# Optimization experiments

Measured on AMD Instinct MI355X. Metric: run time of the kernel, lower is better.

The kernel has to match this reference:

```python
import jax, jax.numpy as jnp
import numpy as np


def setup_inputs() -> dict:
    key = jax.random.key(0)
    k0, k1, k2, k3, k4 = jax.random.split(key, 5)
    feat0 = jax.random.normal(k0, (32, 256, 56, 56), dtype=jnp.float32)
    feat1 = jax.random.normal(k1, (32, 512, 28, 28), dtype=jnp.float32)
    feat2 = jax.random.normal(k2, (32, 1024, 14, 14), dtype=jnp.float32)
    feat3 = jax.random.normal(k3, (32, 2048, 7, 7), dtype=jnp.float32)
    # Conv2d(3840 -> 1024, kernel_size=1, bias=False): weight [emb, C_total]
    conv_w = jax.random.normal(k4, (1024, 3840), dtype=jnp.float32) * 0.02
    return {"feat0": feat0, "feat1": feat1, "feat2": feat2, "feat3": feat3, "conv_w": conv_w}


def reference(feat0, feat1, feat2, feat3, conv_w):
    # Target spatial size = earliest (largest) level.
    Ht, Wt = feat0.shape[2], feat0.shape[3]

    def up_mean(f):
        # Bilinear upsample (torch Upsample align_corners=False == jax 'bilinear'
        # half-pixel resize), then spatial mean per channel.  Because the 1x1
        # conv and global avg-pool are linear, pooling each upsampled level
        # first and applying the conv on the pooled vector is exactly the
        # same math as conv(concat(upsampled)) followed by avg-pool.
        B, C = f.shape[0], f.shape[1]
        up = jax.image.resize(f, (B, C, Ht, Wt), method='bilinear')  # [B,C,Ht,Wt]
        return jnp.mean(up, axis=(2, 3))  # [B,C]

    v = jnp.concatenate([up_mean(f) for f in (feat0, feat1, feat2, feat3)], axis=1)  # [B, 3840]
    # 1x1 conv (no bias) on pooled vector == GEMM with conv weight, then squeeze.
    return v @ conv_w.T  # [B, emb]
```

## Files before the change

kernel.cpp:

```cpp
#include <hip/hip_runtime.h>


#define AS1(p) ((const __attribute__((address_space(1))) void*)(p))
#define AS3(p) ((__attribute__((address_space(3))) void*)(p))

__global__ __launch_bounds__(256) void pool_kernel(
    const float* __restrict__ f0, const float* __restrict__ f1,
    const float* __restrict__ f2, const float* __restrict__ f3,
    float* __restrict__ v)
{
    __shared__ float l[12544];
    int bid = blockIdx.x, t = threadIdx.x;
    int wave = t >> 6, lane = t & 63;

    const float* base;
    if (bid < 2048)      base = f0 + (size_t)bid * 12544;
    else if (bid < 3072) base = f1 + (size_t)(bid - 2048) * 12544;
    else if (bid < 3584) base = f2 + (size_t)(bid - 3072) * 12544;
    else                 base = f3 + (size_t)(bid - 3584) * 12544;

    {
        const float* g = base + wave * 3136;
        float* ld = l + wave * 3136;
        #pragma unroll
        for (int r = 0; r < 12; ++r) {
            __builtin_amdgcn_global_load_lds(
                AS1(g + r * 256 + lane * 4), AS3(ld + r * 256), 16, 0, 0);
        }
        if (lane < 16) {
            __builtin_amdgcn_global_load_lds(
                AS1(g + 3072 + lane * 4), AS3(ld + 3072), 16, 0, 0);
        }
    }
    asm volatile("s_waitcnt vmcnt(0)" ::: "memory");
    __syncthreads();

    const float* seg = l + t * 49;
    float s = 0.f;
    #pragma unroll
    for (int i = 0; i < 49; ++i) s += seg[i];

    if (bid < 2048) {
        #pragma unroll
        for (int o = 32; o; o >>= 1) s += __shfl_xor(s, o);
        if (lane == 0) {
            int q = bid * 4 + wave;
            v[(q >> 8) * 3840 + (q & 255)] = s * (1.f / 3136.f);
        }
    } else if (bid < 3072) {
        s += __shfl_xor(s, 8); s += __shfl_xor(s, 4);
        s += __shfl_xor(s, 2); s += __shfl_xor(s, 1);
        if ((t & 15) == 0) {
            int q = (bid - 2048) * 16 + (t >> 4);
            v[(q >> 9) * 3840 + 256 + (q & 511)] = s * (1.f / 784.f);
        }
    } else if (bid < 3584) {
        s += __shfl_xor(s, 2); s += __shfl_xor(s, 1);
        if ((t & 3) == 0) {
            int q = (bid - 3072) * 64 + (t >> 2);
            v[(q >> 10) * 3840 + 768 + (q & 1023)] = s * (1.f / 196.f);
        }
    } else {
        int q = (bid - 3584) * 256 + t;
        v[(q >> 11) * 3840 + 1792 + (q & 2047)] = s * (1.f / 49.f);
    }
}

#define KT 120

__global__ __launch_bounds__(256) void gemm_kernel(
    const float* __restrict__ v, const float* __restrict__ W,
    float* __restrict__ partials)
{
    __shared__ float vs[32][124];
    __shared__ float wsh[64][124];
    int t = threadIdx.x;
    int et = blockIdx.x & 15, ks = blockIdx.x >> 4;
    int e0 = et << 6, k0 = ks * KT;

    {
        float4 tmp[7];
        int row[7], c4[7];
        #pragma unroll
        for (int i = 0; i < 7; ++i) {
            int f = t + (i << 8);
            row[i] = f / 30; c4[i] = f % 30;
            tmp[i] = *(const float4*)&W[(size_t)(e0 + row[i]) * 3840 + k0 + c4[i] * 4];
        }
        float4 tail; int rowt = 0, c4t = 0;
        if (t < 128) {
            int f = t + 1792;
            rowt = f / 30; c4t = f % 30;
            tail = *(const float4*)&W[(size_t)(e0 + rowt) * 3840 + k0 + c4t * 4];
        }
        #pragma unroll
        for (int i = 0; i < 7; ++i)
            *(float4*)&wsh[row[i]][c4[i] * 4] = tmp[i];
        if (t < 128)
            *(float4*)&wsh[rowt][c4t * 4] = tail;
    }
    {
        float4 tmp[3];
        int row[3], c4[3];
        #pragma unroll
        for (int i = 0; i < 3; ++i) {
            int f = t + (i << 8);
            row[i] = f / 30; c4[i] = f % 30;
            tmp[i] = *(const float4*)&v[row[i] * 3840 + k0 + c4[i] * 4];
        }
        float4 tail; int rowt = 0, c4t = 0;
        if (t < 192) {
            int f = t + 768;
            rowt = f / 30; c4t = f % 30;
            tail = *(const float4*)&v[rowt * 3840 + k0 + c4t * 4];
        }
        #pragma unroll
        for (int i = 0; i < 3; ++i)
            *(float4*)&vs[row[i]][c4[i] * 4] = tmp[i];
        if (t < 192)
            *(float4*)&vs[rowt][c4t * 4] = tail;
    }
    __syncthreads();

    int bg = t >> 5, eg = t & 31;
    int b0 = bg << 2;
    float acc[4][2] = {};
    #pragma unroll 5
    for (int k = 0; k < KT; k += 4) {
        float4 vv[4], ww[2];
        #pragma unroll
        for (int i = 0; i < 4; ++i) vv[i] = *(const float4*)&vs[b0 + i][k];
        #pragma unroll
        for (int j = 0; j < 2; ++j) ww[j] = *(const float4*)&wsh[eg + (j << 5)][k];
        #pragma unroll
        for (int i = 0; i < 4; ++i)
            #pragma unroll
            for (int j = 0; j < 2; ++j)
                acc[i][j] += vv[i].x * ww[j].x + vv[i].y * ww[j].y +
                             vv[i].z * ww[j].z + vv[i].w * ww[j].w;
    }

    float* pout = partials + (size_t)ks * 32768 + (size_t)b0 * 1024 + e0 + eg;
    #pragma unroll
    for (int i = 0; i < 4; ++i)
        #pragma unroll
        for (int j = 0; j < 2; ++j)
            pout[i * 1024 + (j << 5)] = acc[i][j];
}

__global__ __launch_bounds__(256) void reduce_kernel(
    const float* __restrict__ partials, float* __restrict__ out)
{
    int idx = blockIdx.x * 256 + threadIdx.x;
    float s0 = 0.f, s1 = 0.f, s2 = 0.f, s3 = 0.f;
    #pragma unroll
    for (int sp = 0; sp < 32; sp += 4) {
        s0 += partials[(sp + 0) * 32768 + idx];
        s1 += partials[(sp + 1) * 32768 + idx];
        s2 += partials[(sp + 2) * 32768 + idx];
        s3 += partials[(sp + 3) * 32768 + idx];
    }
    out[idx] = (s0 + s1) + (s2 + s3);
}

extern "C" void kernel_launch(void* const* d_in, const int* in_sizes, int n_in,
                              void* d_out, int out_size, void* d_ws, size_t ws_size,
                              hipStream_t stream)
{
    const float* f0 = (const float*)d_in[0];
    const float* f1 = (const float*)d_in[1];
    const float* f2 = (const float*)d_in[2];
    const float* f3 = (const float*)d_in[3];
    const float* W  = (const float*)d_in[4];
    float* out = (float*)d_out;

    float* v        = (float*)d_ws;
    float* partials = v + 32 * 3840;

    pool_kernel<<<3840, 256, 0, stream>>>(f0, f1, f2, f3, v);
    gemm_kernel<<<512, 256, 0, stream>>>(v, W, partials);
    reduce_kernel<<<128, 256, 0, stream>>>(partials, out);
}
```

Before: 233.9 us.

## Make pooling kernel persistent with double-buffered LDS prefetch of channel chunks

Replaces the one-shot pooling kernel with a persistent grid of 1536 blocks. Each block walks 10 chunks of 3136 floats, prefetching the next chunk into a second LDS buffer with async global-to-LDS loads while it reduces the current one. This cuts the LDS footprint per block roughly in half, which should allow more resident blocks per CU, and it overlaps loads with the reduction. In exchange, the level-0 path now needs a cross-wave reduction through LDS plus a block barrier, and the reduction mapping becomes more complex.

```diff
diff --git a/kernel.cpp b/kernel.cpp
--- a/kernel.cpp
+++ b/kernel.cpp
@@ -9,60 +9,77 @@
     const float* __restrict__ f2, const float* __restrict__ f3,
     float* __restrict__ v)
 {
-    __shared__ float l[12544];
-    int bid = blockIdx.x, t = threadIdx.x;
-    int wave = t >> 6, lane = t & 63;
-
-    const float* base;
-    if (bid < 2048)      base = f0 + (size_t)bid * 12544;
-    else if (bid < 3072) base = f1 + (size_t)(bid - 2048) * 12544;
-    else if (bid < 3584) base = f2 + (size_t)(bid - 3072) * 12544;
-    else                 base = f3 + (size_t)(bid - 3584) * 12544;
-
-    {
-        const float* g = base + wave * 3136;
-        float* ld = l + wave * 3136;
-        #pragma unroll
-        for (int r = 0; r < 12; ++r) {
+    __shared__ float l[2 * 3136 + 8];
+    int t = threadIdx.x, w = t >> 6, lane = t & 63;
+    float* warr = l + 6272;
+
+    int c0 = blockIdx.x;
+
+    auto stage = [&](int c, int buf) {
+        const float* base;
+        if (c < 8192)       base = f0 + (size_t)c * 3136;
+        else if (c < 12288) base = f1 + (size_t)(c - 8192) * 3136;
+        else if (c < 14336) base = f2 + (size_t)(c - 12288) * 3136;
+        else                base = f3 + (size_t)(c - 14336) * 3136;
+        const float* g = base + w * 784;
+        float* ld = l + buf * 3136 + w * 784;
+        #pragma unroll
+        for (int r = 0; r < 3; ++r)
             __builtin_amdgcn_global_load_lds(
                 AS1(g + r * 256 + lane * 4), AS3(ld + r * 256), 16, 0, 0);
-        }
-        if (lane < 16) {
+        if (lane < 4)
             __builtin_amdgcn_global_load_lds(
-                AS1(g + 3072 + lane * 4), AS3(ld + 3072), 16, 0, 0);
-        }
-    }
-    asm volatile("s_waitcnt vmcnt(0)" ::: "memory");
-    __syncthreads();
-
-    const float* seg = l + t * 49;
-    float s = 0.f;
-    #pragma unroll
-    for (int i = 0; i < 49; ++i) s += seg[i];
-
-    if (bid < 2048) {
-        #pragma unroll
-        for (int o = 32; o; o >>= 1) s += __shfl_xor(s, o);
-        if (lane == 0) {
-            int q = bid * 4 + wave;
-            v[(q >> 8) * 3840 + (q & 255)] = s * (1.f / 3136.f);
-        }
-    } else if (bid < 3072) {
-        s += __shfl_xor(s, 8); s += __shfl_xor(s, 4);
-        s += __shfl_xor(s, 2); s += __shfl_xor(s, 1);
-        if ((t & 15) == 0) {
-            int q = (bid - 2048) * 16 + (t >> 4);
-            v[(q >> 9) * 3840 + 256 + (q & 511)] = s * (1.f / 784.f);
-        }
-    } else if (bid < 3584) {
-        s += __shfl_xor(s, 2); s += __shfl_xor(s, 1);
-        if ((t & 3) == 0) {
-            int q = (bid - 3072) * 64 + (t >> 2);
-            v[(q >> 10) * 3840 + 768 + (q & 1023)] = s * (1.f / 196.f);
-        }
-    } else {
-        int q = (bid - 3584) * 256 + t;
-        v[(q >> 11) * 3840 + 1792 + (q & 2047)] = s * (1.f / 49.f);
+                AS1(g + 768 + lane * 4), AS3(ld + 768), 16, 0, 0);
+    };
+
+    stage(c0, 0);
+    #pragma unroll 1
+    for (int i = 0; i < 10; ++i) {
+        int c = c0 + 1536 * i;
+        if (i < 9) {
+            stage(c0 + 1536 * (i + 1), (i + 1) & 1);
+            asm volatile("s_waitcnt vmcnt(4)" ::: "memory");
+        } else {
+            asm volatile("s_waitcnt vmcnt(0)" ::: "memory");
+        }
+
+        const float* ldb = l + (i & 1) * 3136 + w * 784;
+        const float* seg = ldb + (lane >> 2) * 49 + (lane & 3) * 12;
+        float s = 0.f;
+        #pragma unroll
+        for (int k = 0; k < 12; ++k) s += seg[k];
+        if ((lane & 3) == 3) s += seg[12];
+        s += __shfl_xor(s, 1); s += __shfl_xor(s, 2);
+
+        if (c < 8192) {
+            s += __shfl_xor(s, 4);  s += __shfl_xor(s, 8);
+            s += __shfl_xor(s, 16); s += __shfl_xor(s, 32);
+            if (lane == 0) warr[(i & 1) * 4 + w] = s;
+            __syncthreads();
+            if (t == 0) {
+                const float* wa = warr + (i & 1) * 4;
+                v[(c >> 8) * 3840 + (c & 255)] =
+                    (wa[0] + wa[1] + wa[2] + wa[3]) * (1.f / 3136.f);
+            }
+        } else if (c < 12288) {
+            s += __shfl_xor(s, 4);  s += __shfl_xor(s, 8);
+            s += __shfl_xor(s, 16); s += __shfl_xor(s, 32);
+            if (lane == 0) {
+                int q = (c - 8192) * 4 + w;
+                v[(q >> 9) * 3840 + 256 + (q & 511)] = s * (1.f / 784.f);
+            }
+        } else if (c < 14336) {
+            s += __shfl_xor(s, 4); s += __shfl_xor(s, 8);
+            if ((lane & 15) == 0) {
+                int q = (c - 12288) * 16 + w * 4 + (lane >> 4);
+                v[(q >> 10) * 3840 + 768 + (q & 1023)] = s * (1.f / 196.f);
+            }
+        } else {
+            if ((lane & 3) == 0) {
+                int q = (c - 14336) * 64 + w * 16 + (lane >> 2);
+                v[(q >> 11) * 3840 + 1792 + (q & 2047)] = s * (1.f / 49.f);
+            }
+        }
     }
 }
 
@@ -177,7 +194,7 @@
     float* v        = (float*)d_ws;
     float* partials = v + 32 * 3840;
 
-    pool_kernel<<<3840, 256, 0, stream>>>(f0, f1, f2, f3, v);
+    pool_kernel<<<1536, 256, 0, stream>>>(f0, f1, f2, f3, v);
     gemm_kernel<<<512, 256, 0, stream>>>(v, W, partials);
     reduce_kernel<<<128, 256, 0, stream>>>(partials, out);
 }
```

Result: no change. 235.9 us (+0.9%).

## Replace LDS staging in pooling kernel with direct register loads

Applied to the files above, without the earlier changes.

The pooling kernel no longer stages each 12544-float block through LDS with global_load_lds. For levels 0 and 1, each wave loads one 3136-float chunk as float4 values straight into registers. Level-1 channels are split into four per-lane partial sums and written back as a single float4. For levels 2 and 3, each thread reads its 49-element channel segment directly from global memory. Removing the 50 KB of shared memory per block should allow more blocks per CU, at the cost of strided per-thread loads on the small levels and higher register use.

```diff
diff --git a/kernel.cpp b/kernel.cpp
--- a/kernel.cpp
+++ b/kernel.cpp
@@ -1,68 +1,79 @@
 #include <hip/hip_runtime.h>
 
 
-#define AS1(p) ((const __attribute__((address_space(1))) void*)(p))
-#define AS3(p) ((__attribute__((address_space(3))) void*)(p))
+__device__ __forceinline__ float s4(float4 a) { return (a.x + a.y) + (a.z + a.w); }
 
 __global__ __launch_bounds__(256) void pool_kernel(
     const float* __restrict__ f0, const float* __restrict__ f1,
     const float* __restrict__ f2, const float* __restrict__ f3,
     float* __restrict__ v)
 {
-    __shared__ float l[12544];
-    int bid = blockIdx.x, t = threadIdx.x;
-    int wave = t >> 6, lane = t & 63;
+    int t = threadIdx.x, w = t >> 6, lane = t & 63;
+    int bid = blockIdx.x;
 
-    const float* base;
-    if (bid < 2048)      base = f0 + (size_t)bid * 12544;
-    else if (bid < 3072) base = f1 + (size_t)(bid - 2048) * 12544;
-    else if (bid < 3584) base = f2 + (size_t)(bid - 3072) * 12544;
-    else                 base = f3 + (size_t)(bid - 3584) * 12544;
+    if (bid < 3072) {
+        int chunk = bid * 4 + w;
+        const float* base = (chunk < 8192)
+            ? f0 + (size_t)chunk * 3136
+            : f1 + (size_t)(chunk - 8192) * 3136;
+        const float4* p = (const float4*)base;
+        float4 r[12];
+        #pragma unroll
+        for (int i = 0; i < 12; ++i) r[i] = p[lane + (i << 6)];
+        float4 tl = make_float4(0.f, 0.f, 0.f, 0.f);
+        if (lane < 16) tl = p[768 + lane];
 
-    {
-        const float* g = base + wave * 3136;
-        float* ld = l + wave * 3136;
-        #pragma unroll
-        for (int r = 0; r < 12; ++r) {
-            __builtin_amdgcn_global_load_lds(
-                AS1(g + r * 256 + lane * 4), AS3(ld + r * 256), 16, 0, 0);
-        }
-        if (lane < 16) {
-            __builtin_amdgcn_global_load_lds(
-                AS1(g + 3072 + lane * 4), AS3(ld + 3072), 16, 0, 0);
-        }
-    }
-    asm volatile("s_waitcnt vmcnt(0)" ::: "memory");
-    __syncthreads();
-
-    const float* seg = l + t * 49;
-    float s = 0.f;
-    #pragma unroll
-    for (int i = 0; i < 49; ++i) s += seg[i];
-
-    if (bid < 2048) {
-        #pragma unroll
-        for (int o = 32; o; o >>= 1) s += __shfl_xor(s, o);
-        if (lane == 0) {
-            int q = bid * 4 + wave;
-            v[(q >> 8) * 3840 + (q & 255)] = s * (1.f / 3136.f);
-        }
-    } else if (bid < 3072) {
-        s += __shfl_xor(s, 8); s += __shfl_xor(s, 4);
-        s += __shfl_xor(s, 2); s += __shfl_xor(s, 1);
-        if ((t & 15) == 0) {
-            int q = (bid - 2048) * 16 + (t >> 4);
-            v[(q >> 9) * 3840 + 256 + (q & 511)] = s * (1.f / 784.f);
-        }
-    } else if (bid < 3584) {
-        s += __shfl_xor(s, 2); s += __shfl_xor(s, 1);
-        if ((t & 3) == 0) {
-            int q = (bid - 3072) * 64 + (t >> 2);
-            v[(q >> 10) * 3840 + 768 + (q & 1023)] = s * (1.f / 196.f);
+        if (chunk < 8192) {
+            float s = 0.f;
+            #pragma unroll
+            for (int i = 0; i < 12; ++i) s += s4(r[i]);
+            s += s4(tl);
+            #pragma unroll
+            for (int o = 32; o; o >>= 1) s += __shfl_xor(s, o);
+            if (lane == 0)
+                v[(chunk >> 8) * 3840 + (chunk & 255)] = s * (1.f / 3136.f);
+        } else {
+            float a0 = s4(r[0]) + s4(r[1]) + s4(r[2]) + (lane <  4 ? s4(r[3]) : 0.f);
+            float a1 = (lane <  4 ? 0.f : s4(r[3])) + s4(r[4]) + s4(r[5])
+                     + (lane <  8 ? s4(r[6]) : 0.f);
+            float a2 = (lane <  8 ? 0.f : s4(r[6])) + s4(r[7]) + s4(r[8])
+                     + (lane < 12 ? s4(r[9]) : 0.f);
+            float a3 = (lane < 12 ? 0.f : s4(r[9])) + s4(r[10]) + s4(r[11]) + s4(tl);
+            #pragma unroll
+            for (int o = 32; o; o >>= 1) {
+                a0 += __shfl_xor(a0, o); a1 += __shfl_xor(a1, o);
+                a2 += __shfl_xor(a2, o); a3 += __shfl_xor(a3, o);
+            }
+            if (lane == 0) {
+                int q = (chunk - 8192) * 4;
+                float4 res = make_float4(a0, a1, a2, a3);
+                *(float4*)&v[(q >> 9) * 3840 + 256 + (q & 511)] =
+                    make_float4(res.x * (1.f / 784.f), res.y * (1.f / 784.f),
+                                res.z * (1.f / 784.f), res.w * (1.f / 784.f));
+            }
         }
     } else {
-        int q = (bid - 3584) * 256 + t;
-        v[(q >> 11) * 3840 + 1792 + (q & 2047)] = s * (1.f / 49.f);
+        int seg = (bid - 3072) * 256 + t;
+        const float* sp = (seg < 131072)
+            ? f2 + (size_t)seg * 49
+            : f3 + (size_t)(seg - 131072) * 49;
+        float x[49];
+        #pragma unroll
+        for (int i = 0; i < 49; ++i) x[i] = sp[i];
+        float s = 0.f;
+        #pragma unroll
+        for (int i = 0; i < 48; i += 2) s += x[i] + x[i + 1];
+        s += x[48];
+        if (seg < 131072) {
+            s += __shfl_xor(s, 1); s += __shfl_xor(s, 2);
+            if ((lane & 3) == 0) {
+                int q = seg >> 2;
+                v[(q >> 10) * 3840 + 768 + (q & 1023)] = s * (1.f / 196.f);
+            }
+        } else {
+            int q = seg - 131072;
+            v[(q >> 11) * 3840 + 1792 + (q & 2047)] = s * (1.f / 49.f);
+        }
     }
 }
 
```

Result: no change. 233.4 us (-0.2%).
